# Performance work log

Hardware: AMD Instinct MI355X
Metric: run time of the kernel (lower is better)

## Reference

```python
import jax, jax.numpy as jnp
import numpy as np

B = 256          # batch
H = 1024         # conditioning_size (dec_hid_dim)
D = 256          # gst_dim
G = 32           # num_gst
C = 16           # num_cells
O = 256          # output_size


def setup_inputs() -> dict:
    key = jax.random.key(0)
    ks = jax.random.split(key, 7)
    hidden = jax.random.normal(ks[0], (B, H), dtype=jnp.float32)
    # per-cell embedding tables: nn.Embedding(num_gst, gst_dim) stacked over cells
    gst_emb = jax.random.normal(ks[1], (C, G, D), dtype=jnp.float32)
    # per-cell Linear(gst_dim + cond, cond): weight [H, H + D] (torch [out, in]), bias [H]
    attn_w = jax.random.normal(ks[2], (C, H, H + D), dtype=jnp.float32) * 0.02
    attn_b = jax.random.normal(ks[3], (C, H), dtype=jnp.float32) * 0.02
    # per-cell v: Parameter(torch.rand(cond))
    v = jax.random.uniform(ks[4], (C, H), dtype=jnp.float32)
    # out Linear(gst_dim, output_size)
    out_w = jax.random.normal(ks[5], (O, D), dtype=jnp.float32) * 0.02
    out_b = jax.random.normal(ks[6], (O,), dtype=jnp.float32) * 0.02
    return {"hidden": hidden, "gst_emb": gst_emb, "attn_w": attn_w,
            "attn_b": attn_b, "v": v, "out_w": out_w, "out_b": out_b}


def reference(hidden, gst_emb, attn_w, attn_b, v, out_w, out_b):
    # Original concatenates (hidden, encoder_outputs) along features; split the
    # linear weight accordingly instead of materializing the concat.
    w_hid = attn_w[:, :, :H]        # [C, H, H]
    w_enc = attn_w[:, :, H:]        # [C, H, D]
    # embedding lookup of arange(G) == the table rows themselves (same for all batch)
    enc = gst_emb                   # [C, G, D]
    hid_part = jnp.einsum('bh,coh->bco', hidden, w_hid)     # [B, C, Ho]
    enc_part = jnp.einsum('cgd,cod->cgo', enc, w_enc)       # [C, G, Ho]
    energy = jnp.tanh(hid_part[:, :, None, :] + enc_part[None]
                      + attn_b[None, :, None, :])           # [B, C, G, Ho]
    scores = jnp.einsum('bcgh,ch->bcg', energy, v)          # [B, C, G]
    attention = jax.nn.softmax(scores, axis=-1)             # softmax over num_gst
    weighted = jnp.einsum('bcg,cgd->bcd', attention, enc)   # [B, C, D]
    att_cat = attention.reshape(B, C * G)                   # torch.cat(att_list, dim=1)
    pooled = jnp.mean(weighted, axis=1)                     # [B, D]
    out = pooled @ out_w.T + out_b                          # [B, O]
    return (att_cat, out)
```

## Files before the change

### kernel.cpp

```cpp
#include <hip/hip_runtime.h>
#include <hip/hip_bf16.h>

#define B_  256
#define H_  1024
#define D_  256
#define G_  32
#define C_  16
#define O_  256
#define HD_ 1280
#define N1_ 16384
#define RS_ 36

typedef __attribute__((ext_vector_type(8))) short short8;
typedef __attribute__((ext_vector_type(4))) short s16x4;
typedef __attribute__((ext_vector_type(4))) float f32x4;

#define MFMA16(a, b, c) __builtin_amdgcn_mfma_f32_16x16x32_bf16((a), (b), (c), 0, 0, 0)

__device__ __forceinline__ float tanh_c(float x) {
    float y = __expf(2.f * x);
    float t = 1.f - 2.f * __builtin_amdgcn_rcpf(y + 1.f);
    return fminf(fmaxf(t, -0.99999994f), 0.99999994f);
}

__device__ __forceinline__ short bfhi(float x) {
    return (short)(__float_as_uint(x) >> 16);
}
__device__ __forceinline__ short bflo(float x) {
    float fhi = __uint_as_float(__float_as_uint(x) & 0xFFFF0000u);
    return (short)(__float_as_uint(x - fhi) >> 16);
}

__device__ __forceinline__ void split4(const float4 v, s16x4& hi, s16x4& lo) {
    hi[0] = bfhi(v.x); lo[0] = bflo(v.x);
    hi[1] = bfhi(v.y); lo[1] = bflo(v.y);
    hi[2] = bfhi(v.z); lo[2] = bflo(v.z);
    hi[3] = bfhi(v.w); lo[3] = bflo(v.w);
}

__global__ __launch_bounds__(512) void gemm1_kernel(
    const float* __restrict__ hidden, const float* __restrict__ attn_w,
    const float* __restrict__ attn_b, float* __restrict__ hp)
{
    __shared__ short AsH[128 * RS_];
    __shared__ short AsL[128 * RS_];
    __shared__ short BsH[128 * RS_];
    __shared__ short BsL[128 * RS_];

    const int tid  = threadIdx.x;
    const int wave = tid >> 6, lane = tid & 63;
    const int m0 = blockIdx.x * 128;
    const int n0 = blockIdx.y * 128;
    const int wm = (wave >> 2) * 64;
    const int wn = (wave & 3) * 32;
    const int l16 = lane & 15;
    const int lk  = (lane >> 4) * 8;

    f32x4 acc[4][2];
    #pragma unroll
    for (int mi = 0; mi < 4; ++mi)
        #pragma unroll
        for (int ni = 0; ni < 2; ++ni)
            acc[mi][ni] = f32x4{0.f, 0.f, 0.f, 0.f};

    int rr[2], cc[2];
    #pragma unroll
    for (int i = 0; i < 2; ++i) {
        const int chunk = tid + i * 512;
        rr[i] = chunk >> 3;
        cc[i] = (chunk & 7) * 4;
    }

    const float* pA0 = hidden + (m0 + rr[0]) * H_ + cc[0];
    const float* pA1 = hidden + (m0 + rr[1]) * H_ + cc[1];
    const float* pB0 = attn_w + (size_t)(n0 + rr[0]) * HD_ + cc[0];
    const float* pB1 = attn_w + (size_t)(n0 + rr[1]) * HD_ + cc[1];

    float4 va[2], vb[2];
    va[0] = *(const float4*)(pA0);
    va[1] = *(const float4*)(pA1);
    vb[0] = *(const float4*)(pB0);
    vb[1] = *(const float4*)(pB1);

    for (int k0 = 0; k0 < H_; k0 += 32) {
        __syncthreads();
        #pragma unroll
        for (int i = 0; i < 2; ++i) {
            s16x4 h, l;
            split4(va[i], h, l);
            *(s16x4*)(AsH + rr[i] * RS_ + cc[i]) = h;
            *(s16x4*)(AsL + rr[i] * RS_ + cc[i]) = l;
            split4(vb[i], h, l);
            *(s16x4*)(BsH + rr[i] * RS_ + cc[i]) = h;
            *(s16x4*)(BsL + rr[i] * RS_ + cc[i]) = l;
        }
        __syncthreads();

        if (k0 + 32 < H_) {
            const int kn = k0 + 32;
            va[0] = *(const float4*)(pA0 + kn);
            va[1] = *(const float4*)(pA1 + kn);
            vb[0] = *(const float4*)(pB0 + kn);
            vb[1] = *(const float4*)(pB1 + kn);
        }

        short8 ah[4], al[4], bh[2], bl[2];
        #pragma unroll
        for (int mi = 0; mi < 4; ++mi) {
            ah[mi] = *(const short8*)(AsH + (wm + mi * 16 + l16) * RS_ + lk);
            al[mi] = *(const short8*)(AsL + (wm + mi * 16 + l16) * RS_ + lk);
        }
        #pragma unroll
        for (int ni = 0; ni < 2; ++ni) {
            bh[ni] = *(const short8*)(BsH + (wn + ni * 16 + l16) * RS_ + lk);
            bl[ni] = *(const short8*)(BsL + (wn + ni * 16 + l16) * RS_ + lk);
        }
        #pragma unroll
        for (int mi = 0; mi < 4; ++mi)
            #pragma unroll
            for (int ni = 0; ni < 2; ++ni) {
                acc[mi][ni] = MFMA16(ah[mi], bh[ni], acc[mi][ni]);
                acc[mi][ni] = MFMA16(al[mi], bh[ni], acc[mi][ni]);
                acc[mi][ni] = MFMA16(ah[mi], bl[ni], acc[mi][ni]);
            }
    }

    const int lr = (lane >> 4) * 4;
    #pragma unroll
    for (int mi = 0; mi < 4; ++mi) {
        #pragma unroll
        for (int ni = 0; ni < 2; ++ni) {
            const int col  = n0 + wn + ni * 16 + l16;
            const float bias = attn_b[col];
            float* dst = hp + (size_t)(m0 + wm + mi * 16 + lr) * N1_ + col;
            f32x4 vacc = acc[mi][ni];
            dst[0]        = tanh_c(vacc[0] + bias);
            dst[N1_]      = tanh_c(vacc[1] + bias);
            dst[2 * N1_]  = tanh_c(vacc[2] + bias);
            dst[3 * N1_]  = tanh_c(vacc[3] + bias);
        }
    }
}

__global__ __launch_bounds__(256) void gemm2_kernel(
    const float* __restrict__ enc, const float* __restrict__ attn_w,
    float* __restrict__ ep)
{
    const int tid  = threadIdx.x;
    const int wave = tid >> 6, lane = tid & 63;
    const int c  = blockIdx.y;
    const int n0 = blockIdx.x * 64 + wave * 16;
    const int l16 = lane & 15;
    const int lk  = (lane >> 4) * 8;

    f32x4 acc[2];
    acc[0] = f32x4{0.f, 0.f, 0.f, 0.f};
    acc[1] = f32x4{0.f, 0.f, 0.f, 0.f};

    const float* encp = enc + c * (G_ * D_);
    const float* wp   = attn_w + (size_t)c * H_ * HD_ + H_;

    #pragma unroll
    for (int kk = 0; kk < 8; ++kk) {
        const int k0 = kk * 32 + lk;
        short8 ah[2], al[2], bh, bl;
        #pragma unroll
        for (int mi = 0; mi < 2; ++mi) {
            const float* p = encp + (mi * 16 + l16) * D_ + k0;
            s16x4 h0, l0, h1, l1;
            split4(*(const float4*)p, h0, l0);
            split4(*(const float4*)(p + 4), h1, l1);
            ah[mi] = short8{h0[0],h0[1],h0[2],h0[3],h1[0],h1[1],h1[2],h1[3]};
            al[mi] = short8{l0[0],l0[1],l0[2],l0[3],l1[0],l1[1],l1[2],l1[3]};
        }
        {
            const float* p = wp + (size_t)(n0 + l16) * HD_ + k0;
            s16x4 h0, l0, h1, l1;
            split4(*(const float4*)p, h0, l0);
            split4(*(const float4*)(p + 4), h1, l1);
            bh = short8{h0[0],h0[1],h0[2],h0[3],h1[0],h1[1],h1[2],h1[3]};
            bl = short8{l0[0],l0[1],l0[2],l0[3],l1[0],l1[1],l1[2],l1[3]};
        }
        #pragma unroll
        for (int mi = 0; mi < 2; ++mi) {
            acc[mi] = MFMA16(ah[mi], bh, acc[mi]);
            acc[mi] = MFMA16(al[mi], bh, acc[mi]);
            acc[mi] = MFMA16(ah[mi], bl, acc[mi]);
        }
    }

    const int lr = (lane >> 4) * 4;
    #pragma unroll
    for (int mi = 0; mi < 2; ++mi) {
        const int g = mi * 16 + lr;
        const int o = n0 + l16;
        float* dst = ep + (c * G_ + g) * H_ + o;
        f32x4 vacc = acc[mi];
        dst[0]      = tanh_c(vacc[0]);
        dst[H_]     = tanh_c(vacc[1]);
        dst[2 * H_] = tanh_c(vacc[2]);
        dst[3 * H_] = tanh_c(vacc[3]);
    }
}

__global__ __launch_bounds__(256) void attn_kernel(
    const float* __restrict__ hp, const float* __restrict__ ep,
    const float* __restrict__ v, const float* __restrict__ enc,
    float* __restrict__ out, float* __restrict__ wt)
{
    const int c  = blockIdx.x;
    const int b0 = blockIdx.y * 4;
    const int tid  = threadIdx.x;
    const int wave = tid >> 6, lane = tid & 63;

    __shared__ float s_att[4][G_];
    __shared__ float s_sc[G_][4];

    float tav[4][16], vv[16];
    const float* vrow = v + c * H_;
    #pragma unroll
    for (int j = 0; j < 16; ++j) {
        const int o = lane + j * 64;
        vv[j] = vrow[o];
        #pragma unroll
        for (int bi = 0; bi < 4; ++bi)
            tav[bi][j] = hp[(size_t)(b0 + bi) * N1_ + c * H_ + o];
    }

    #pragma unroll
    for (int gg = 0; gg < 8; ++gg) {
        const int g = wave * 8 + gg;
        const float* eprow = ep + (c * G_ + g) * H_;
        float s[4] = {0.f, 0.f, 0.f, 0.f};
        #pragma unroll
        for (int j = 0; j < 16; ++j) {
            const float tb = eprow[lane + j * 64];
            #pragma unroll
            for (int bi = 0; bi < 4; ++bi) {
                const float ta  = tav[bi][j];
                const float den = fmaf(ta, tb, 1.f);
                const float r   = __builtin_amdgcn_rcpf(den);
                s[bi] = fmaf((ta + tb) * r, vv[j], s[bi]);
            }
        }
        #pragma unroll
        for (int off = 32; off > 0; off >>= 1)
            #pragma unroll
            for (int bi = 0; bi < 4; ++bi)
                s[bi] += __shfl_down(s[bi], off, 64);
        if (lane == 0) {
            #pragma unroll
            for (int bi = 0; bi < 4; ++bi)
                s_sc[g][bi] = s[bi];
        }
    }
    __syncthreads();

    if (tid < 128) {
        const int bi = tid >> 5, gl = tid & 31;
        float s = s_sc[gl][bi];
        float m = s;
        #pragma unroll
        for (int off = 16; off > 0; off >>= 1)
            m = fmaxf(m, __shfl_xor(m, off, 32));
        const float e = __expf(s - m);
        float sum = e;
        #pragma unroll
        for (int off = 16; off > 0; off >>= 1)
            sum += __shfl_xor(sum, off, 32);
        const float a = e / sum;
        s_att[bi][gl] = a;
        out[(size_t)(b0 + bi) * (C_ * G_) + c * G_ + gl] = a;
    }
    __syncthreads();

    float w[4] = {0.f, 0.f, 0.f, 0.f};
    const float* encc = enc + c * (G_ * D_) + tid;
    #pragma unroll
    for (int g = 0; g < G_; ++g) {
        const float e = encc[g * D_];
        #pragma unroll
        for (int bi = 0; bi < 4; ++bi)
            w[bi] = fmaf(s_att[bi][g], e, w[bi]);
    }
    #pragma unroll
    for (int bi = 0; bi < 4; ++bi)
        wt[(size_t)((b0 + bi) * C_ + c) * D_ + tid] = w[bi];
}

__global__ __launch_bounds__(256) void out_kernel(
    const float* __restrict__ wt, const float* __restrict__ out_w,
    const float* __restrict__ out_b, float* __restrict__ out)
{
    const int b = blockIdx.x, tid = threadIdx.x;
    __shared__ float pooled[D_];

    float s = 0.f;
    #pragma unroll
    for (int c = 0; c < C_; ++c)
        s += wt[(size_t)(b * C_ + c) * D_ + tid];
    pooled[tid] = s * (1.f / 16.f);
    __syncthreads();

    float acc = out_b[tid];
    const float* wrow = out_w + tid * D_;
    #pragma unroll 8
    for (int dc = 0; dc < 64; ++dc) {
        float4 w4 = *(const float4*)(wrow + dc * 4);
        acc += pooled[dc * 4 + 0] * w4.x;
        acc += pooled[dc * 4 + 1] * w4.y;
        acc += pooled[dc * 4 + 2] * w4.z;
        acc += pooled[dc * 4 + 3] * w4.w;
    }
    out[(size_t)B_ * (C_ * G_) + b * O_ + tid] = acc;
}

extern "C" void kernel_launch(void* const* d_in, const int* in_sizes, int n_in,
                              void* d_out, int out_size, void* d_ws, size_t ws_size,
                              hipStream_t stream) {
    const float* hidden = (const float*)d_in[0];
    const float* enc    = (const float*)d_in[1];
    const float* attn_w = (const float*)d_in[2];
    const float* attn_b = (const float*)d_in[3];
    const float* v      = (const float*)d_in[4];
    const float* out_w  = (const float*)d_in[5];
    const float* out_b  = (const float*)d_in[6];
    float* out = (float*)d_out;

    float* hp = (float*)d_ws;
    float* ep = hp + (size_t)B_ * N1_;
    float* wt = ep + (size_t)C_ * G_ * H_;

    gemm1_kernel<<<dim3(2, 128), 512, 0, stream>>>(hidden, attn_w, attn_b, hp);
    gemm2_kernel<<<dim3(16, C_), 256, 0, stream>>>(enc, attn_w, ep);
    attn_kernel<<<dim3(C_, B_ / 4), 256, 0, stream>>>(hp, ep, v, enc, out, wt);
    out_kernel<<<B_, 256, 0, stream>>>(wt, out_w, out_b, out);
}
```

Baseline: 208.1 us.

## Pre-split hidden into bf16 hi/lo and load A fragments directly from global

Adds a small kernel that splits the hidden activations into bf16 hi/lo arrays once, so gemm1 no longer redoes that split in every block. gemm1 now reads A fragments straight from global memory into registers with a one-step prefetch, dropping the A shared-memory tiles. Blocks shrink to 256 threads with a 64x128 tile, which doubles the grid and loads more of the weight matrix per thread into LDS. This costs an extra kernel launch and hi/lo workspace, and A is now re-read from global by each wave in the block rather than shared through LDS.

```diff
diff --git a/kernel.cpp b/kernel.cpp
--- a/kernel.cpp
+++ b/kernel.cpp
@@ -38,21 +38,30 @@
     hi[3] = bfhi(v.w); lo[3] = bflo(v.w);
 }
 
-__global__ __launch_bounds__(512) void gemm1_kernel(
-    const float* __restrict__ hidden, const float* __restrict__ attn_w,
+__global__ __launch_bounds__(256) void splitA_kernel(
+    const float* __restrict__ h, short* __restrict__ hi, short* __restrict__ lo)
+{
+    const int idx = (blockIdx.x * 256 + threadIdx.x) * 4;
+    float4 v = *(const float4*)(h + idx);
+    s16x4 a, b;
+    split4(v, a, b);
+    *(s16x4*)(hi + idx) = a;
+    *(s16x4*)(lo + idx) = b;
+}
+
+__global__ __launch_bounds__(256) void gemm1_kernel(
+    const short* __restrict__ Ahi, const short* __restrict__ Alo,
+    const float* __restrict__ attn_w,
     const float* __restrict__ attn_b, float* __restrict__ hp)
 {
-    __shared__ short AsH[128 * RS_];
-    __shared__ short AsL[128 * RS_];
     __shared__ short BsH[128 * RS_];
     __shared__ short BsL[128 * RS_];
 
     const int tid  = threadIdx.x;
     const int wave = tid >> 6, lane = tid & 63;
-    const int m0 = blockIdx.x * 128;
+    const int m0 = blockIdx.x * 64;
     const int n0 = blockIdx.y * 128;
-    const int wm = (wave >> 2) * 64;
-    const int wn = (wave & 3) * 32;
+    const int wn = wave * 32;
     const int l16 = lane & 15;
     const int lk  = (lane >> 4) * 8;
 
@@ -63,33 +72,40 @@
         for (int ni = 0; ni < 2; ++ni)
             acc[mi][ni] = f32x4{0.f, 0.f, 0.f, 0.f};
 
-    int rr[2], cc[2];
-    #pragma unroll
-    for (int i = 0; i < 2; ++i) {
-        const int chunk = tid + i * 512;
+    int rr[4], cc[4];
+    #pragma unroll
+    for (int i = 0; i < 4; ++i) {
+        const int chunk = tid + i * 256;
         rr[i] = chunk >> 3;
         cc[i] = (chunk & 7) * 4;
     }
-
-    const float* pA0 = hidden + (m0 + rr[0]) * H_ + cc[0];
-    const float* pA1 = hidden + (m0 + rr[1]) * H_ + cc[1];
     const float* pB0 = attn_w + (size_t)(n0 + rr[0]) * HD_ + cc[0];
     const float* pB1 = attn_w + (size_t)(n0 + rr[1]) * HD_ + cc[1];
-
-    float4 va[2], vb[2];
-    va[0] = *(const float4*)(pA0);
-    va[1] = *(const float4*)(pA1);
+    const float* pB2 = attn_w + (size_t)(n0 + rr[2]) * HD_ + cc[2];
+    const float* pB3 = attn_w + (size_t)(n0 + rr[3]) * HD_ + cc[3];
+
+    const short* pAh = Ahi + (m0 + l16) * H_ + lk;
+    const short* pAl = Alo + (m0 + l16) * H_ + lk;
+
+    float4 vb[4];
     vb[0] = *(const float4*)(pB0);
     vb[1] = *(const float4*)(pB1);
-
+    vb[2] = *(const float4*)(pB2);
+    vb[3] = *(const float4*)(pB3);
+
+    short8 ahc[4], alc[4], ahn[4], aln[4];
+    #pragma unroll
+    for (int mi = 0; mi < 4; ++mi) {
+        ahc[mi] = *(const short8*)(pAh + mi * 16 * H_);
+        alc[mi] = *(const short8*)(pAl + mi * 16 * H_);
+    }
+
+    #pragma unroll 2
     for (int k0 = 0; k0 < H_; k0 += 32) {
         __syncthreads();
         #pragma unroll
-        for (int i = 0; i < 2; ++i) {
+        for (int i = 0; i < 4; ++i) {
             s16x4 h, l;
-            split4(va[i], h, l);
-            *(s16x4*)(AsH + rr[i] * RS_ + cc[i]) = h;
-            *(s16x4*)(AsL + rr[i] * RS_ + cc[i]) = l;
             split4(vb[i], h, l);
             *(s16x4*)(BsH + rr[i] * RS_ + cc[i]) = h;
             *(s16x4*)(BsL + rr[i] * RS_ + cc[i]) = l;
@@ -98,18 +114,18 @@
 
         if (k0 + 32 < H_) {
             const int kn = k0 + 32;
-            va[0] = *(const float4*)(pA0 + kn);
-            va[1] = *(const float4*)(pA1 + kn);
             vb[0] = *(const float4*)(pB0 + kn);
             vb[1] = *(const float4*)(pB1 + kn);
-        }
-
-        short8 ah[4], al[4], bh[2], bl[2];
-        #pragma unroll
-        for (int mi = 0; mi < 4; ++mi) {
-            ah[mi] = *(const short8*)(AsH + (wm + mi * 16 + l16) * RS_ + lk);
-            al[mi] = *(const short8*)(AsL + (wm + mi * 16 + l16) * RS_ + lk);
-        }
+            vb[2] = *(const float4*)(pB2 + kn);
+            vb[3] = *(const float4*)(pB3 + kn);
+            #pragma unroll
+            for (int mi = 0; mi < 4; ++mi) {
+                ahn[mi] = *(const short8*)(pAh + mi * 16 * H_ + kn);
+                aln[mi] = *(const short8*)(pAl + mi * 16 * H_ + kn);
+            }
+        }
+
+        short8 bh[2], bl[2];
         #pragma unroll
         for (int ni = 0; ni < 2; ++ni) {
             bh[ni] = *(const short8*)(BsH + (wn + ni * 16 + l16) * RS_ + lk);
@@ -119,10 +135,16 @@
         for (int mi = 0; mi < 4; ++mi)
             #pragma unroll
             for (int ni = 0; ni < 2; ++ni) {
-                acc[mi][ni] = MFMA16(ah[mi], bh[ni], acc[mi][ni]);
-                acc[mi][ni] = MFMA16(al[mi], bh[ni], acc[mi][ni]);
-                acc[mi][ni] = MFMA16(ah[mi], bl[ni], acc[mi][ni]);
+                acc[mi][ni] = MFMA16(ahc[mi], bh[ni], acc[mi][ni]);
+                acc[mi][ni] = MFMA16(alc[mi], bh[ni], acc[mi][ni]);
+                acc[mi][ni] = MFMA16(ahc[mi], bl[ni], acc[mi][ni]);
             }
+
+        #pragma unroll
+        for (int mi = 0; mi < 4; ++mi) {
+            ahc[mi] = ahn[mi];
+            alc[mi] = aln[mi];
+        }
     }
 
     const int lr = (lane >> 4) * 4;
@@ -132,7 +154,7 @@
         for (int ni = 0; ni < 2; ++ni) {
             const int col  = n0 + wn + ni * 16 + l16;
             const float bias = attn_b[col];
-            float* dst = hp + (size_t)(m0 + wm + mi * 16 + lr) * N1_ + col;
+            float* dst = hp + (size_t)(m0 + mi * 16 + lr) * N1_ + col;
             f32x4 vacc = acc[mi][ni];
             dst[0]        = tanh_c(vacc[0] + bias);
             dst[N1_]      = tanh_c(vacc[1] + bias);
@@ -330,8 +352,11 @@
     float* hp = (float*)d_ws;
     float* ep = hp + (size_t)B_ * N1_;
     float* wt = ep + (size_t)C_ * G_ * H_;
-
-    gemm1_kernel<<<dim3(2, 128), 512, 0, stream>>>(hidden, attn_w, attn_b, hp);
+    short* Ahi = (short*)(wt + (size_t)B_ * C_ * D_);
+    short* Alo = Ahi + (size_t)B_ * H_;
+
+    splitA_kernel<<<B_ * H_ / 1024, 256, 0, stream>>>(hidden, Ahi, Alo);
+    gemm1_kernel<<<dim3(4, 128), 256, 0, stream>>>(Ahi, Alo, attn_w, attn_b, hp);
     gemm2_kernel<<<dim3(16, C_), 256, 0, stream>>>(enc, attn_w, ep);
     attn_kernel<<<dim3(C_, B_ / 4), 256, 0, stream>>>(hp, ep, v, enc, out, wt);
     out_kernel<<<B_, 256, 0, stream>>>(wt, out_w, out_b, out);
```

Result: slower. 240.2 us (+15.4%).
